# Performance work log

Hardware: AMD Instinct MI355X
Metric: run time of the kernel (lower is better)

The kernel has to match this reference:

```python
import jax, jax.numpy as jnp
import numpy as np

FE = 16
L = 32 * FE            # 512 input spatial size
K5 = 5 + 8 * (FE - 1)  # 125, C5 kernel so output is 1x1
F6_OUT = 16 * 24 * FE * FE  # 98304

# LeNet-5 sparse connection table for C3, read off the slicing in ConvC3.forward
C3_GROUPS = [
    [0, 1, 2], [1, 2, 3], [2, 3, 4], [3, 4, 5], [4, 5, 0], [5, 0, 1],
    [0, 1, 2, 3], [1, 2, 3, 4], [2, 3, 4, 5], [3, 4, 5, 0], [4, 5, 0, 1], [5, 0, 1, 2],
    [0, 1, 3, 4], [1, 2, 4, 5], [0, 2, 3, 5], [0, 1, 2, 3, 4, 5],
]

def c3_mask():
    m = np.zeros((16, 6, 1, 1), np.float32)
    for o, g in enumerate(C3_GROUPS):
        m[o, g, 0, 0] = 1.0
    return jnp.asarray(m)

_C3_MASK = c3_mask()

def conv2d(x, w, b):
    # x: (C,H,W) unbatched; w: (O,I,kh,kw); VALID, stride 1
    y = jax.lax.conv_general_dilated(x[None], w, (1, 1), 'VALID',
                                     dimension_numbers=('NCHW', 'OIHW', 'NCHW'))[0]
    return y + b[:, None, None]

def avgpool2(x):
    C, H, W = x.shape
    return x.reshape(C, H // 2, 2, W // 2, 2).mean(axis=(2, 4))

def setup_inputs() -> dict:
    key = jax.random.key(0)
    ks = jax.random.split(key, 6)
    x = jax.random.normal(ks[0], (1, L, L), dtype=jnp.float32)
    W1 = jax.random.normal(ks[1], (6, 1, 5, 5), dtype=jnp.float32) * 0.1
    b1 = jnp.zeros((6,), jnp.float32)
    W3 = jax.random.normal(ks[2], (16, 6, 5, 5), dtype=jnp.float32) * 0.1
    b3 = jnp.zeros((16,), jnp.float32)
    W5 = jax.random.normal(ks[3], (120, 16, K5, K5), dtype=jnp.float32) * 0.01
    b5 = jnp.zeros((120,), jnp.float32)
    W6 = jax.random.normal(ks[4], (F6_OUT, 120), dtype=jnp.float32) * 0.05
    b6 = jnp.zeros((F6_OUT,), jnp.float32)
    W7 = jax.random.normal(ks[5], (54, F6_OUT), dtype=jnp.float32) * 0.01
    b7 = jnp.zeros((54,), jnp.float32)
    return {"x": x, "W1": W1, "b1": b1, "W3": W3, "b3": b3,
            "W5": W5, "b5": b5, "W6": W6, "b6": b6, "W7": W7, "b7": b7}

def reference(x, W1, b1, W3, b3, W5, b5, W6, b6, W7, b7):
    relu = jax.nn.relu
    h = relu(conv2d(x, W1, b1))            # (6, 508, 508)
    h = avgpool2(h)                        # (6, 254, 254)
    # C3: 16 tiny sparse-connected 5x5 convs fused into one masked dense conv
    h = relu(conv2d(h, W3 * _C3_MASK, b3)) # (16, 250, 250)
    h = avgpool2(h)                        # (16, 125, 125)
    h = relu(conv2d(h, W5, b5))            # (120, 1, 1)
    h = h.reshape(-1, 120)                 # (1, 120)
    h = relu(h @ W6.T + b6)                # (1, 98304)
    return h @ W7.T + b7                   # (1, 54)
```

## Files before the change

### kernel.cpp

```cpp
#include <hip/hip_runtime.h>

#define P1 254
#define P2 125
#define C5_K 250000
#define C5_K4 62500
#define C5_CHUNK_F4 1250
#define F6_OUT 98304
#define F7_K4 24576
#define F7_CHUNK_F4 1024

#define WS_H2 0
#define WS_H4 400000
#define WS_C5 650000
#define WS_H6 650128

__global__ __launch_bounds__(256) void c1_s2_kernel(const float* __restrict__ x,
        const float* __restrict__ W1, const float* __restrict__ b1,
        float* __restrict__ h2,
        const float* __restrict__ b5, const float* __restrict__ b7,
        float* __restrict__ c5acc, float* __restrict__ out) {
    if (blockIdx.x == 0) {
        int t = threadIdx.x;
        if (t < 120) c5acc[t] = b5[t];
        if (t >= 128 && t < 182) out[t - 128] = b7[t - 128];
    }
    int t = blockIdx.x * 256 + threadIdx.x;
    const int total = 6 * P1 * P1;
    if (t >= total) return;
    int c  = t / (P1 * P1);
    int r  = t % (P1 * P1);
    int y  = r / P1, x0 = r % P1;

    float w[25];
    #pragma unroll
    for (int k = 0; k < 25; ++k) w[k] = W1[c * 25 + k];

    float p[6][6];
    const float2* xin2 = (const float2*)(x + (2 * y) * 512 + 2 * x0);
    #pragma unroll
    for (int i = 0; i < 6; ++i) {
        float2 a0 = xin2[i * 256 + 0];
        float2 a1 = xin2[i * 256 + 1];
        float2 a2 = xin2[i * 256 + 2];
        p[i][0] = a0.x; p[i][1] = a0.y; p[i][2] = a1.x;
        p[i][3] = a1.y; p[i][4] = a2.x; p[i][5] = a2.y;
    }

    float bias = b1[c];
    float s = 0.f;
    #pragma unroll
    for (int dy = 0; dy < 2; ++dy)
        #pragma unroll
        for (int dx = 0; dx < 2; ++dx) {
            float a = bias;
            #pragma unroll
            for (int kh = 0; kh < 5; ++kh)
                #pragma unroll
                for (int kw = 0; kw < 5; ++kw)
                    a = fmaf(p[dy + kh][dx + kw], w[kh * 5 + kw], a);
            s += fmaxf(a, 0.f);
        }
    h2[t] = 0.25f * s;
}

__global__ __launch_bounds__(256) void c3_s4_kernel(const float* __restrict__ h2,
        const float* __restrict__ W3, const float* __restrict__ b3,
        float* __restrict__ h4) {
    const unsigned char MASK[16] = {7,14,28,56,49,35,15,30,60,57,51,39,27,54,45,63};
    int t = blockIdx.x * 256 + threadIdx.x;
    const int total = 16 * P2 * P2;
    if (t >= total) return;
    int o  = t / (P2 * P2);
    int r  = t % (P2 * P2);
    int y  = r / P2, x0 = r % P2;

    float a00, a01, a10, a11;
    a00 = a01 = a10 = a11 = b3[o];
    unsigned m = MASK[o];

    for (int i = 0; i < 6; ++i) {
        if (!((m >> i) & 1)) continue;
        const float2* hp2 = (const float2*)(h2 + i * P1 * P1 + (2 * y) * P1 + 2 * x0);
        const float* wp = W3 + (o * 6 + i) * 25;
        float w[25];
        #pragma unroll
        for (int k = 0; k < 25; ++k) w[k] = wp[k];
        float p[6][6];
        #pragma unroll
        for (int ii = 0; ii < 6; ++ii) {
            float2 a0 = hp2[ii * 127 + 0];
            float2 a1 = hp2[ii * 127 + 1];
            float2 a2 = hp2[ii * 127 + 2];
            p[ii][0] = a0.x; p[ii][1] = a0.y; p[ii][2] = a1.x;
            p[ii][3] = a1.y; p[ii][4] = a2.x; p[ii][5] = a2.y;
        }
        #pragma unroll
        for (int kh = 0; kh < 5; ++kh)
            #pragma unroll
            for (int kw = 0; kw < 5; ++kw) {
                float wv = w[kh * 5 + kw];
                a00 = fmaf(p[kh][kw],         wv, a00);
                a01 = fmaf(p[kh][kw + 1],     wv, a01);
                a10 = fmaf(p[kh + 1][kw],     wv, a10);
                a11 = fmaf(p[kh + 1][kw + 1], wv, a11);
            }
    }
    h4[t] = 0.25f * (fmaxf(a00, 0.f) + fmaxf(a01, 0.f) + fmaxf(a10, 0.f) + fmaxf(a11, 0.f));
}

__device__ __forceinline__ float block_reduce_256(float v) {
    #pragma unroll
    for (int off = 32; off > 0; off >>= 1) v += __shfl_down(v, off, 64);
    __shared__ float s[4];
    int lane = threadIdx.x & 63, wv = threadIdx.x >> 6;
    if (lane == 0) s[wv] = v;
    __syncthreads();
    return s[0] + s[1] + s[2] + s[3];
}

__global__ __launch_bounds__(256) void c5_kernel(const float* __restrict__ h4,
        const float* __restrict__ W5, float* __restrict__ c5acc) {
    int row = blockIdx.y;
    const float4* wr = (const float4*)(W5 + (size_t)row * C5_K);
    const float4* hv = (const float4*)h4;
    int start = blockIdx.x * C5_CHUNK_F4;
    int end   = start + C5_CHUNK_F4;
    float s = 0.f;
    for (int i = start + (int)threadIdx.x; i < end; i += 256) {
        float4 w = wr[i], h = hv[i];
        s = fmaf(w.x, h.x, s); s = fmaf(w.y, h.y, s);
        s = fmaf(w.z, h.z, s); s = fmaf(w.w, h.w, s);
    }
    s = block_reduce_256(s);
    if (threadIdx.x == 0) atomicAdd(&c5acc[row], s);
}

#define F6_RPB 128
#define F6_STRIDE 124
__global__ __launch_bounds__(256) void f6_kernel(const float* __restrict__ c5acc,
        const float* __restrict__ W6, const float* __restrict__ b6,
        float* __restrict__ h6) {
    __shared__ float ws6[F6_RPB * F6_STRIDE];
    __shared__ float h5s[120];
    int tid = threadIdx.x;
    int base = blockIdx.x * F6_RPB;
    if (tid < 120) h5s[tid] = fmaxf(c5acc[tid], 0.f);
    const float4* src = (const float4*)(W6 + (size_t)base * 120);
    #pragma unroll
    for (int i = 0; i < 15; ++i) {
        int f4 = tid + i * 256;
        float4 v = src[f4];
        int flat = f4 * 4;
        int row = flat / 120;
        int col = flat - row * 120;
        *(float4*)&ws6[row * F6_STRIDE + col] = v;
    }
    __syncthreads();
    int row  = tid >> 1;
    int half = tid & 1;
    const float4* wr4 = (const float4*)&ws6[row * F6_STRIDE + half * 60];
    const float4* hh4 = (const float4*)&h5s[half * 60];
    float a = 0.f;
    #pragma unroll
    for (int j = 0; j < 15; ++j) {
        float4 w = wr4[j], h = hh4[j];
        a = fmaf(w.x, h.x, a); a = fmaf(w.y, h.y, a);
        a = fmaf(w.z, h.z, a); a = fmaf(w.w, h.w, a);
    }
    a += __shfl_xor(a, 1, 64);
    if (half == 0) {
        int o = base + row;
        h6[o] = fmaxf(a + b6[o], 0.f);
    }
}

__global__ __launch_bounds__(256) void f7_kernel(const float* __restrict__ h6,
        const float* __restrict__ W7, float* __restrict__ out) {
    int row = blockIdx.y;
    const float4* wr = (const float4*)(W7 + (size_t)row * (F7_K4 * 4));
    const float4* hv = (const float4*)h6;
    int start = blockIdx.x * F7_CHUNK_F4;
    int end   = start + F7_CHUNK_F4;
    float s = 0.f;
    for (int i = start + (int)threadIdx.x; i < end; i += 256) {
        float4 w = wr[i], h = hv[i];
        s = fmaf(w.x, h.x, s); s = fmaf(w.y, h.y, s);
        s = fmaf(w.z, h.z, s); s = fmaf(w.w, h.w, s);
    }
    s = block_reduce_256(s);
    if (threadIdx.x == 0) atomicAdd(&out[row], s);
}

extern "C" void kernel_launch(void* const* d_in, const int* in_sizes, int n_in,
                              void* d_out, int out_size, void* d_ws, size_t ws_size,
                              hipStream_t stream) {
    const float* x  = (const float*)d_in[0];
    const float* W1 = (const float*)d_in[1];
    const float* b1 = (const float*)d_in[2];
    const float* W3 = (const float*)d_in[3];
    const float* b3 = (const float*)d_in[4];
    const float* W5 = (const float*)d_in[5];
    const float* b5 = (const float*)d_in[6];
    const float* W6 = (const float*)d_in[7];
    const float* b6 = (const float*)d_in[8];
    const float* W7 = (const float*)d_in[9];
    const float* b7 = (const float*)d_in[10];
    float* out = (float*)d_out;
    float* ws  = (float*)d_ws;

    float* h2 = ws + WS_H2;
    float* h4 = ws + WS_H4;
    float* c5 = ws + WS_C5;
    float* h6 = ws + WS_H6;

    {
        int total = 6 * P1 * P1;
        c1_s2_kernel<<<(total + 255) / 256, 256, 0, stream>>>(x, W1, b1, h2, b5, b7, c5, out);
    }
    {
        int total = 16 * P2 * P2;
        c3_s4_kernel<<<(total + 255) / 256, 256, 0, stream>>>(h2, W3, b3, h4);
    }
    c5_kernel<<<dim3(C5_K4 / C5_CHUNK_F4, 120), 256, 0, stream>>>(h4, W5, c5);
    f6_kernel<<<F6_OUT / F6_RPB, 256, 0, stream>>>(c5, W6, b6, h6);
    f7_kernel<<<dim3(F7_K4 / F7_CHUNK_F4, 54), 256, 0, stream>>>(h6, W7, out);
}
```

Before: 288.0 us.

## Fuse F6 and F7 into one kernel with last-block partial reduction

Merges the F6 and F7 fully connected layers into a single kernel. Each block keeps its 128 F6 outputs in shared memory and computes partial F7 dot products against the matching W7 columns, writing them to a workspace buffer. The last block to finish, found with an atomic counter, sums the partials and adds the bias. This removes the h6 round trip through global memory and one launch. W7 is now read as 54 separate 512-byte row slices per block, so those reads are less coalesced, and a serial final reduction over 768 partials is added.

```diff
diff --git a/kernel.cpp b/kernel.cpp
--- a/kernel.cpp
+++ b/kernel.cpp
@@ -6,23 +6,25 @@
 #define C5_K4 62500
 #define C5_CHUNK_F4 1250
 #define F6_OUT 98304
-#define F7_K4 24576
-#define F7_CHUNK_F4 1024
-
-#define WS_H2 0
-#define WS_H4 400000
-#define WS_C5 650000
-#define WS_H6 650128
+#define F6_RPB 128
+#define F6_NBLK (F6_OUT / F6_RPB)
+#define F6_STRIDE 124
+
+#define WS_H2   0
+#define WS_H4   400000
+#define WS_C5   650000
+#define WS_PART 800000
+#define WS_CNT  860000
 
 __global__ __launch_bounds__(256) void c1_s2_kernel(const float* __restrict__ x,
         const float* __restrict__ W1, const float* __restrict__ b1,
         float* __restrict__ h2,
-        const float* __restrict__ b5, const float* __restrict__ b7,
-        float* __restrict__ c5acc, float* __restrict__ out) {
+        const float* __restrict__ b5,
+        float* __restrict__ c5acc, unsigned int* __restrict__ counter) {
     if (blockIdx.x == 0) {
         int t = threadIdx.x;
         if (t < 120) c5acc[t] = b5[t];
-        if (t >= 128 && t < 182) out[t - 128] = b7[t - 128];
+        if (t == 128) counter[0] = 0u;
     }
     int t = blockIdx.x * 256 + threadIdx.x;
     const int total = 6 * P1 * P1;
@@ -135,13 +137,15 @@
     if (threadIdx.x == 0) atomicAdd(&c5acc[row], s);
 }
 
-#define F6_RPB 128
-#define F6_STRIDE 124
-__global__ __launch_bounds__(256) void f6_kernel(const float* __restrict__ c5acc,
+__global__ __launch_bounds__(256) void f6f7_kernel(const float* __restrict__ c5acc,
         const float* __restrict__ W6, const float* __restrict__ b6,
-        float* __restrict__ h6) {
+        const float* __restrict__ W7, const float* __restrict__ b7,
+        float* __restrict__ part, unsigned int* __restrict__ counter,
+        float* __restrict__ out) {
     __shared__ float ws6[F6_RPB * F6_STRIDE];
     __shared__ float h5s[120];
+    __shared__ float h6s[F6_RPB];
+    __shared__ unsigned int lastflag;
     int tid = threadIdx.x;
     int base = blockIdx.x * F6_RPB;
     if (tid < 120) h5s[tid] = fmaxf(c5acc[tid], 0.f);
@@ -156,39 +160,50 @@
         *(float4*)&ws6[row * F6_STRIDE + col] = v;
     }
     __syncthreads();
-    int row  = tid >> 1;
-    int half = tid & 1;
-    const float4* wr4 = (const float4*)&ws6[row * F6_STRIDE + half * 60];
-    const float4* hh4 = (const float4*)&h5s[half * 60];
-    float a = 0.f;
-    #pragma unroll
-    for (int j = 0; j < 15; ++j) {
-        float4 w = wr4[j], h = hh4[j];
-        a = fmaf(w.x, h.x, a); a = fmaf(w.y, h.y, a);
-        a = fmaf(w.z, h.z, a); a = fmaf(w.w, h.w, a);
-    }
-    a += __shfl_xor(a, 1, 64);
-    if (half == 0) {
-        int o = base + row;
-        h6[o] = fmaxf(a + b6[o], 0.f);
-    }
-}
-
-__global__ __launch_bounds__(256) void f7_kernel(const float* __restrict__ h6,
-        const float* __restrict__ W7, float* __restrict__ out) {
-    int row = blockIdx.y;
-    const float4* wr = (const float4*)(W7 + (size_t)row * (F7_K4 * 4));
-    const float4* hv = (const float4*)h6;
-    int start = blockIdx.x * F7_CHUNK_F4;
-    int end   = start + F7_CHUNK_F4;
-    float s = 0.f;
-    for (int i = start + (int)threadIdx.x; i < end; i += 256) {
-        float4 w = wr[i], h = hv[i];
-        s = fmaf(w.x, h.x, s); s = fmaf(w.y, h.y, s);
-        s = fmaf(w.z, h.z, s); s = fmaf(w.w, h.w, s);
-    }
-    s = block_reduce_256(s);
-    if (threadIdx.x == 0) atomicAdd(&out[row], s);
+    {
+        int row  = tid >> 1;
+        int half = tid & 1;
+        const float4* wr4 = (const float4*)&ws6[row * F6_STRIDE + half * 60];
+        const float4* hh4 = (const float4*)&h5s[half * 60];
+        float a = 0.f;
+        #pragma unroll
+        for (int j = 0; j < 15; ++j) {
+            float4 w = wr4[j], h = hh4[j];
+            a = fmaf(w.x, h.x, a); a = fmaf(w.y, h.y, a);
+            a = fmaf(w.z, h.z, a); a = fmaf(w.w, h.w, a);
+        }
+        a += __shfl_xor(a, 1, 64);
+        if (half == 0) h6s[row] = fmaxf(a + b6[base + row], 0.f);
+    }
+    __syncthreads();
+    {
+        int wv = tid >> 6, lane = tid & 63;
+        for (int o = wv; o < 54; o += 4) {
+            const float* w7r = W7 + (size_t)o * F6_OUT + base;
+            float p = fmaf(w7r[lane], h6s[lane], w7r[lane + 64] * h6s[lane + 64]);
+            #pragma unroll
+            for (int off = 32; off > 0; off >>= 1) p += __shfl_down(p, off, 64);
+            if (lane == 0) part[(size_t)blockIdx.x * 64 + o] = p;
+        }
+    }
+    __threadfence();
+    __syncthreads();
+    if (tid == 0) {
+        unsigned int old = atomicAdd(counter, 1u);
+        lastflag = (old == F6_NBLK - 1) ? 1u : 0u;
+    }
+    __syncthreads();
+    if (!lastflag) return;
+    __threadfence();
+    if (tid < 216) {
+        int o = tid >> 2, q = tid & 3;
+        float s = 0.f;
+        for (int b = q; b < F6_NBLK; b += 4)
+            s += part[(size_t)b * 64 + o];
+        s += __shfl_down(s, 1, 64);
+        s += __shfl_down(s, 2, 64);
+        if (q == 0) out[o] = b7[o] + s;
+    }
 }
 
 extern "C" void kernel_launch(void* const* d_in, const int* in_sizes, int n_in,
@@ -211,17 +226,17 @@
     float* h2 = ws + WS_H2;
     float* h4 = ws + WS_H4;
     float* c5 = ws + WS_C5;
-    float* h6 = ws + WS_H6;
+    float* part = ws + WS_PART;
+    unsigned int* counter = (unsigned int*)(ws + WS_CNT);
 
     {
         int total = 6 * P1 * P1;
-        c1_s2_kernel<<<(total + 255) / 256, 256, 0, stream>>>(x, W1, b1, h2, b5, b7, c5, out);
+        c1_s2_kernel<<<(total + 255) / 256, 256, 0, stream>>>(x, W1, b1, h2, b5, c5, counter);
     }
     {
         int total = 16 * P2 * P2;
         c3_s4_kernel<<<(total + 255) / 256, 256, 0, stream>>>(h2, W3, b3, h4);
     }
     c5_kernel<<<dim3(C5_K4 / C5_CHUNK_F4, 120), 256, 0, stream>>>(h4, W5, c5);
-    f6_kernel<<<F6_OUT / F6_RPB, 256, 0, stream>>>(c5, W6, b6, h6);
-    f7_kernel<<<dim3(F7_K4 / F7_CHUNK_F4, 54), 256, 0, stream>>>(h6, W7, out);
-}
+    f6f7_kernel<<<F6_NBLK, 256, 0, stream>>>(c5, W6, b6, W7, b7, part, counter, out);
+}
```

After: 399.0 us. +38.5%, slower.
